# Performance work log

Hardware: AMD Instinct MI355X
Metric: run time of the kernel (lower is better)

Reference implementation:

```python
import jax, jax.numpy as jnp
import numpy as np

B, T, C = 2, 2048, 1024
H = 16
D = C // H  # head_dim = 64
SCALE = D ** -0.5


def setup_inputs() -> dict:
    key = jax.random.key(0)
    ks = jax.random.split(key, 5)
    s = 0.02
    return {
        "x": jax.random.normal(ks[0], (B, T, C), dtype=jnp.float32),
        "w_qkv": jax.random.normal(ks[1], (C, 3 * C), dtype=jnp.float32) * s,
        "b_qkv": jnp.zeros((3 * C,), dtype=jnp.float32),
        "w_proj": jax.random.normal(ks[2], (C, C), dtype=jnp.float32) * s,
        "b_proj": jnp.zeros((C,), dtype=jnp.float32),
    }


def reference(x, w_qkv, b_qkv, w_proj, b_proj):
    Bx, Tx, Cx = x.shape
    qkv = x @ w_qkv + b_qkv                      # [B,T,3C]
    q, k, v = jnp.split(qkv, 3, axis=-1)
    # [B,T,C] -> [B,H,T,D]
    q = q.reshape(Bx, Tx, H, D).transpose(0, 2, 1, 3)
    k = k.reshape(Bx, Tx, H, D).transpose(0, 2, 1, 3)
    v = v.reshape(Bx, Tx, H, D).transpose(0, 2, 1, 3)
    attn = jnp.einsum('bhqd,bhkd->bhqk', q, k) * SCALE
    causal = jnp.tril(jnp.ones((Tx, Tx), dtype=bool))
    attn = jnp.where(causal[None, None], attn, -jnp.inf)
    attn = jax.nn.softmax(attn, axis=-1)
    out = jnp.einsum('bhqk,bhkd->bhqd', attn, v)  # [B,H,T,D]
    out = out.transpose(0, 2, 1, 3).reshape(Bx, Tx, Cx)
    return out @ w_proj + b_proj
```

## Files before the change

### kernel.cpp

```cpp
#include <hip/hip_runtime.h>
#include <hip/hip_bf16.h>
#include <math.h>

#define T_SEQ 2048
#define NHEAD 16
#define HDIM  64
#define CDIM  1024
#define KDIM  1024
#define SCALE_L2E 0.1803368801111204f

typedef __attribute__((ext_vector_type(8))) short bf16x8;
typedef __attribute__((ext_vector_type(4))) float f32x4;
typedef __attribute__((ext_vector_type(16))) float f32x16;
typedef __attribute__((ext_vector_type(8))) unsigned short u16x8;
typedef __attribute__((ext_vector_type(4))) unsigned int u32x4;

__device__ __forceinline__ unsigned short f2bf(float f) {
    unsigned int u = __builtin_bit_cast(unsigned int, f);
    u += 0x7fffu + ((u >> 16) & 1u);
    return (unsigned short)(u >> 16);
}
__device__ __forceinline__ unsigned int cvt_pk_bf16(float lo, float hi_) {
    unsigned int r;
    asm("v_cvt_pk_bf16_f32 %0, %1, %2" : "=v"(r) : "v"(lo), "v"(hi_));
    return r;
}
__device__ __forceinline__ void pl32swap(unsigned int &a, unsigned int &b) {
    asm("v_permlane32_swap_b32 %0, %1" : "+v"(a), "+v"(b));
}
__device__ __forceinline__ void gld16(const unsigned short* g, unsigned short* l) {
    __builtin_amdgcn_global_load_lds(
        (const __attribute__((address_space(1))) unsigned int*)g,
        (__attribute__((address_space(3))) unsigned int*)l,
        16, 0, 0);
}

__global__ __launch_bounds__(256) void prep_all(
    const float* __restrict__ x,  unsigned short* __restrict__ Xb,
    const float* __restrict__ wq, unsigned short* __restrict__ Wqt,
    const float* __restrict__ wp, unsigned short* __restrict__ Wpt)
{
    __shared__ unsigned short Ls[64][72];
    const int bid = blockIdx.x;
    if (bid < 2048) {
        size_t i = ((size_t)bid * 256 + threadIdx.x) * 8;
        float4 a = *(const float4*)(x + i);
        float4 b = *(const float4*)(x + i + 4);
        u32x4 o;
        o[0] = cvt_pk_bf16(a.x, a.y);
        o[1] = cvt_pk_bf16(a.z, a.w);
        o[2] = cvt_pk_bf16(b.x, b.y);
        o[3] = cvt_pk_bf16(b.z, b.w);
        *(u32x4*)(Xb + i) = o;
        return;
    }
    const float* W; unsigned short* Wt; int NC, n0, k0;
    if (bid < 2048 + 768) {
        int b = bid - 2048;
        W = wq; Wt = Wqt; NC = 3072; n0 = (b % 48) * 64; k0 = (b / 48) * 64;
    } else {
        int b = bid - 2816;
        W = wp; Wt = Wpt; NC = 1024; n0 = (b % 16) * 64; k0 = (b / 16) * 64;
    }
    const int t = threadIdx.x;
    {
        int kr = t >> 2, nc = (t & 3) * 16;
        #pragma unroll
        for (int j = 0; j < 4; j++) {
            float4 v = *(const float4*)(W + (size_t)(k0 + kr) * NC + n0 + nc + j * 4);
            Ls[nc + j*4 + 0][kr] = f2bf(v.x);
            Ls[nc + j*4 + 1][kr] = f2bf(v.y);
            Ls[nc + j*4 + 2][kr] = f2bf(v.z);
            Ls[nc + j*4 + 3][kr] = f2bf(v.w);
        }
    }
    __syncthreads();
    {
        int nr = t >> 2, kc = (t & 3) * 16;
        u16x8 o0 = *(const u16x8*)&Ls[nr][kc];
        u16x8 o1 = *(const u16x8*)&Ls[nr][kc + 8];
        *(u16x8*)(Wt + (size_t)(n0 + nr) * KDIM + k0 + kc)     = o0;
        *(u16x8*)(Wt + (size_t)(n0 + nr) * KDIM + k0 + kc + 8) = o1;
    }
}

template<int NC, int EPI>
__global__ __launch_bounds__(256) void gemm_k(
    const unsigned short* __restrict__ A, const unsigned short* __restrict__ Wt,
    const float* __restrict__ bias, float* __restrict__ Of,
    unsigned short* __restrict__ Qb, unsigned short* __restrict__ Kb,
    unsigned short* __restrict__ Vt)
{
    __shared__ unsigned short As[128 * 64];
    __shared__ unsigned short Bs[128 * 64];

    const int tid  = threadIdx.x;
    const int lane = tid & 63;
    const int wid  = tid >> 6;
    const int m0 = blockIdx.x * 128;
    const int n0 = blockIdx.y * 128;
    const int wm = (wid >> 1) * 64;
    const int wn = (wid & 1) * 64;
    const int rl = lane & 15;

    const int r8 = lane >> 3, s8 = lane & 7;
    const int swzs = (s8 ^ r8) * 8;

    f32x4 acc[4][4] = {};

    for (int k0 = 0; k0 < KDIM; k0 += 64) {
        #pragma unroll
        for (int c = 0; c < 4; c++) {
            int row = (wid << 5) + (c << 3) + r8;
            gld16(A  + (size_t)(m0 + row) * KDIM + k0 + swzs, &As[(size_t)((wid<<5)+(c<<3)) * 64]);
            gld16(Wt + (size_t)(n0 + row) * KDIM + k0 + swzs, &Bs[(size_t)((wid<<5)+(c<<3)) * 64]);
        }
        __syncthreads();
        #pragma unroll
        for (int kc = 0; kc < 2; kc++) {
            const int sb = kc * 4 + (lane >> 4);
            bf16x8 af[4], bfr[4];
            #pragma unroll
            for (int f = 0; f < 4; f++) {
                int sw = (sb ^ (rl & 7)) * 8;
                af[f]  = *(const bf16x8*)&As[(wm + f*16 + rl) * 64 + sw];
                bfr[f] = *(const bf16x8*)&Bs[(wn + f*16 + rl) * 64 + sw];
            }
            __builtin_amdgcn_s_setprio(1);
            #pragma unroll
            for (int i = 0; i < 4; i++)
                #pragma unroll
                for (int j = 0; j < 4; j++)
                    acc[i][j] = __builtin_amdgcn_mfma_f32_16x16x32_bf16(af[i], bfr[j], acc[i][j], 0, 0, 0);
            __builtin_amdgcn_s_setprio(0);
        }
        __syncthreads();
    }

    #pragma unroll
    for (int j = 0; j < 4; j++) {
        int gn = n0 + wn + j*16 + rl;
        float bv = bias[gn];
        #pragma unroll
        for (int i = 0; i < 4; i++) {
            int gm0 = m0 + wm + i*16 + (lane >> 4) * 4;
            #pragma unroll
            for (int r = 0; r < 4; r++) {
                float v = acc[i][j][r] + bv;
                int gm = gm0 + r;
                if (EPI == 0) {
                    int which = gn >> 10;
                    int cw = gn & 1023;
                    int h = cw >> 6, d = cw & 63;
                    int b = gm >> 11, t = gm & 2047;
                    size_t bh = (size_t)(b * NHEAD + h);
                    if (which == 0)      Qb[(bh * T_SEQ + t) * HDIM + d] = f2bf(v * SCALE_L2E);
                    else if (which == 1) Kb[(bh * T_SEQ + t) * HDIM + d] = f2bf(v);
                    else                 Vt[(bh * HDIM + d) * T_SEQ + t] = f2bf(v);
                } else {
                    Of[(size_t)gm * NC + gn] = v;
                }
            }
        }
    }
}

__global__ __launch_bounds__(256, 4) void attn_k(
    const unsigned short* __restrict__ Qb, const unsigned short* __restrict__ Kb,
    const unsigned short* __restrict__ Vt, unsigned short* __restrict__ AO)
{
    __shared__ unsigned short sbuf[4 * 4096];
    __shared__ float mlbuf[2 * 64];

    const int tid  = threadIdx.x;
    const int lane = tid & 63;
    const int w    = tid >> 6;
    const int pair = w >> 1;
    const int par  = w & 1;
    const int bh   = blockIdx.x;
    const int by   = blockIdx.y;
    const int qt   = pair ? (63 - by) : by;
    const int ql   = lane & 31;
    const int hi   = lane >> 5;
    const int qg   = (qt << 5) + ql;

    const unsigned short* Qp = Qb + (size_t)bh * T_SEQ * HDIM;
    const unsigned short* Kp = Kb + (size_t)bh * T_SEQ * HDIM;
    const unsigned short* Vp = Vt + (size_t)bh * HDIM * T_SEQ;

    unsigned short* kbuf = sbuf + w * 4096;
    const char* kbB = (const char*)kbuf;
    const char* vbB = (const char*)(kbuf + 2048);

    const int r8 = lane >> 3, s8 = lane & 7;
    const int key = s8 ^ r8;
    const unsigned short* kSrc = Kp + (size_t)r8 * HDIM + (key << 3);
    const unsigned short* vSrc = Vp + (size_t)((key >> 2) * 32 + r8) * T_SEQ + (key & 3) * 8;

    auto issue_tile = [&](int t) {
        #pragma unroll
        for (int c = 0; c < 4; c++)
            gld16(kSrc + ((size_t)t << 11) + (c << 9), kbuf + (c << 9));
        #pragma unroll
        for (int c = 0; c < 4; c++)
            gld16(vSrc + ((size_t)c << 14) + (t << 5), kbuf + 2048 + (c << 9));
    };

    bf16x8 qf[4];
    #pragma unroll
    for (int dc = 0; dc < 4; dc++)
        qf[dc] = *(const bf16x8*)(Qp + (size_t)qg * HDIM + dc*16 + hi*8);

    float l_run = 0.f;
    f32x16 o0 = {}, o1 = {};

    if (par <= qt) {
        issue_tile(par);
        for (int t = par; t <= qt; t += 2) {
            asm volatile("s_waitcnt vmcnt(0)" ::: "memory");
            __builtin_amdgcn_sched_barrier(0);

            bf16x8 kf[4];
            #pragma unroll
            for (int dc = 0; dc < 4; dc++)
                kf[dc] = *(const bf16x8*)(kbB + ql*128 + (((dc << 1 | hi) ^ (ql & 7)) << 4));
            bf16x8 v00 = *(const bf16x8*)(vbB + ql*128 + (((0 + hi) ^ (ql & 7)) << 4));
            bf16x8 v01 = *(const bf16x8*)(vbB + ql*128 + (((2 + hi) ^ (ql & 7)) << 4));
            bf16x8 v10 = *(const bf16x8*)(vbB + ql*128 + (((4 + hi) ^ (ql & 7)) << 4));
            bf16x8 v11 = *(const bf16x8*)(vbB + ql*128 + (((6 + hi) ^ (ql & 7)) << 4));
            asm volatile("s_waitcnt lgkmcnt(0)" ::: "memory");
            __builtin_amdgcn_sched_barrier(0);

            if (t + 2 <= qt) issue_tile(t + 2);

            f32x16 s = {};
            __builtin_amdgcn_s_setprio(1);
            #pragma unroll
            for (int dc = 0; dc < 4; dc++)
                s = __builtin_amdgcn_mfma_f32_32x32x16_bf16(kf[dc], qf[dc], s, 0, 0, 0);
            __builtin_amdgcn_s_setprio(0);

            float p[16];
            if (t == qt) {
                #pragma unroll
                for (int r = 0; r < 16; r++) {
                    int kv = (t << 5) + (r & 3) + 8 * (r >> 2) + 4 * hi;
                    p[r] = (kv > qg) ? 0.f : exp2f(s[r]);
                }
            } else {
                #pragma unroll
                for (int r = 0; r < 16; r++) p[r] = exp2f(s[r]);
            }
            float r0 = (p[0]  + p[1])  + (p[2]  + p[3]);
            float r1 = (p[4]  + p[5])  + (p[6]  + p[7]);
            float r2 = (p[8]  + p[9])  + (p[10] + p[11]);
            float r3 = (p[12] + p[13]) + (p[14] + p[15]);
            l_run += (r0 + r1) + (r2 + r3);

            unsigned int c[8];
            #pragma unroll
            for (int i = 0; i < 8; i++) c[i] = cvt_pk_bf16(p[2*i], p[2*i+1]);
            pl32swap(c[0], c[2]);  pl32swap(c[1], c[3]);
            pl32swap(c[4], c[6]);  pl32swap(c[5], c[7]);
            u32x4 b0 = {c[0], c[1], c[2], c[3]};
            u32x4 b1 = {c[4], c[5], c[6], c[7]};
            bf16x8 pf0 = __builtin_bit_cast(bf16x8, b0);
            bf16x8 pf1 = __builtin_bit_cast(bf16x8, b1);

            __builtin_amdgcn_s_setprio(1);
            o0 = __builtin_amdgcn_mfma_f32_32x32x16_bf16(v00, pf0, o0, 0, 0, 0);
            o0 = __builtin_amdgcn_mfma_f32_32x32x16_bf16(v01, pf1, o0, 0, 0, 0);
            o1 = __builtin_amdgcn_mfma_f32_32x32x16_bf16(v10, pf0, o1, 0, 0, 0);
            o1 = __builtin_amdgcn_mfma_f32_32x32x16_bf16(v11, pf1, o1, 0, 0, 0);
            __builtin_amdgcn_s_setprio(0);
        }
    }

    __syncthreads();
    float* plf = (float*)(sbuf + pair * 8192);
    if (par == 1) {
        #pragma unroll
        for (int j = 0; j < 4; j++) {
            f32x4 a = { o0[4*j], o0[4*j+1], o0[4*j+2], o0[4*j+3] };
            *(f32x4*)(plf + (size_t)(j*64 + lane) * 4) = a;
        }
        #pragma unroll
        for (int j = 0; j < 4; j++) {
            f32x4 a = { o1[4*j], o1[4*j+1], o1[4*j+2], o1[4*j+3] };
            *(f32x4*)(plf + (size_t)((4+j)*64 + lane) * 4) = a;
        }
        mlbuf[pair * 64 + lane] = l_run;
    }
    __syncthreads();
    if (par == 0) {
        float l_all = l_run + mlbuf[pair * 64 + lane];
        l_all += __shfl_xor(l_all, 32);
        float linv = 1.f / l_all;
        const int b = bh >> 4, h = bh & 15;
        unsigned short* aop = AO + ((size_t)(b * T_SEQ + qg)) * CDIM + h * HDIM;
        #pragma unroll
        for (int qd = 0; qd < 4; qd++) {
            f32x4 x0 = *(const f32x4*)(plf + (size_t)(qd*64 + lane) * 4);
            f32x4 x1 = *(const f32x4*)(plf + (size_t)((4+qd)*64 + lane) * 4);
            uint2 w0, w1;
            w0.x = cvt_pk_bf16((o0[4*qd+0] + x0[0]) * linv, (o0[4*qd+1] + x0[1]) * linv);
            w0.y = cvt_pk_bf16((o0[4*qd+2] + x0[2]) * linv, (o0[4*qd+3] + x0[3]) * linv);
            w1.x = cvt_pk_bf16((o1[4*qd+0] + x1[0]) * linv, (o1[4*qd+1] + x1[1]) * linv);
            w1.y = cvt_pk_bf16((o1[4*qd+2] + x1[2]) * linv, (o1[4*qd+3] + x1[3]) * linv);
            *(uint2*)(aop + qd*8 + hi*4)      = w0;
            *(uint2*)(aop + 32 + qd*8 + hi*4) = w1;
        }
    }
}

extern "C" void kernel_launch(void* const* d_in, const int* in_sizes, int n_in,
                              void* d_out, int out_size, void* d_ws, size_t ws_size,
                              hipStream_t stream) {
    const float* x      = (const float*)d_in[0];
    const float* w_qkv  = (const float*)d_in[1];
    const float* b_qkv  = (const float*)d_in[2];
    const float* w_proj = (const float*)d_in[3];
    const float* b_proj = (const float*)d_in[4];
    float* out = (float*)d_out;

    const size_t MI = (size_t)1 << 20;
    unsigned short* base = (unsigned short*)d_ws;
    unsigned short* Qb  = base;
    unsigned short* Kb  = base + 4*MI;
    unsigned short* Vt  = base + 8*MI;
    unsigned short* Wqt = base + 12*MI;
    unsigned short* Wpt = base + 15*MI;
    unsigned short* Xb  = base + 16*MI;
    unsigned short* AO  = Xb;

    prep_all<<<dim3(3072), 256, 0, stream>>>(x, Xb, w_qkv, Wqt, w_proj, Wpt);
    gemm_k<3072, 0><<<dim3(32, 24), 256, 0, stream>>>(
        Xb, Wqt, b_qkv, nullptr, Qb, Kb, Vt);
    attn_k<<<dim3(32, 32), 256, 0, stream>>>(Qb, Kb, Vt, AO);
    gemm_k<1024, 1><<<dim3(32, 8), 256, 0, stream>>>(
        AO, Wpt, b_proj, out, nullptr, nullptr, nullptr);
}
```

Baseline: 110.0 us.

## Triple-buffer GEMM shared-memory tiles with async prefetch two stages ahead

Replaces the single-buffered K=64 GEMM main loop with a three-slot ring of K=32 shared-memory tiles. Global-to-LDS loads are issued two stages ahead and gated by explicit vmcnt waits and barriers, so memory latency overlaps with MFMA work and one barrier per iteration is removed. The swizzle is re-derived for the 32-wide rows. Each barrier now covers half as much compute, and the hand-written vmcnt accounting has to match the number of loads in flight exactly.

```diff
diff --git a/kernel.cpp b/kernel.cpp
--- a/kernel.cpp
+++ b/kernel.cpp
@@ -91,8 +91,8 @@
     unsigned short* __restrict__ Qb, unsigned short* __restrict__ Kb,
     unsigned short* __restrict__ Vt)
 {
-    __shared__ unsigned short As[128 * 64];
-    __shared__ unsigned short Bs[128 * 64];
+    __shared__ unsigned short As3[3 * 128 * 32];
+    __shared__ unsigned short Bs3[3 * 128 * 32];
 
     const int tid  = threadIdx.x;
     const int lane = tid & 63;
@@ -103,39 +103,56 @@
     const int wn = (wid & 1) * 64;
     const int rl = lane & 15;
 
-    const int r8 = lane >> 3, s8 = lane & 7;
-    const int swzs = (s8 ^ r8) * 8;
+    const int rOff   = lane >> 2;
+    const int srcOff = ((lane & 3) ^ ((lane >> 3) & 3)) * 8;
+
+    auto stage = [&](int t) {
+        const int k0 = t << 5;
+        #pragma unroll
+        for (int i = 0; i < 2; i++) {
+            int rb = (wid << 5) + (i << 4);
+            gld16(A  + (size_t)(m0 + rb + rOff) * KDIM + k0 + srcOff, &As3[(t % 3) * 4096 + rb * 32]);
+            gld16(Wt + (size_t)(n0 + rb + rOff) * KDIM + k0 + srcOff, &Bs3[(t % 3) * 4096 + rb * 32]);
+        }
+    };
 
     f32x4 acc[4][4] = {};
-
-    for (int k0 = 0; k0 < KDIM; k0 += 64) {
-        #pragma unroll
-        for (int c = 0; c < 4; c++) {
-            int row = (wid << 5) + (c << 3) + r8;
-            gld16(A  + (size_t)(m0 + row) * KDIM + k0 + swzs, &As[(size_t)((wid<<5)+(c<<3)) * 64]);
-            gld16(Wt + (size_t)(n0 + row) * KDIM + k0 + swzs, &Bs[(size_t)((wid<<5)+(c<<3)) * 64]);
-        }
-        __syncthreads();
-        #pragma unroll
-        for (int kc = 0; kc < 2; kc++) {
-            const int sb = kc * 4 + (lane >> 4);
-            bf16x8 af[4], bfr[4];
-            #pragma unroll
-            for (int f = 0; f < 4; f++) {
-                int sw = (sb ^ (rl & 7)) * 8;
-                af[f]  = *(const bf16x8*)&As[(wm + f*16 + rl) * 64 + sw];
-                bfr[f] = *(const bf16x8*)&Bs[(wn + f*16 + rl) * 64 + sw];
-            }
-            __builtin_amdgcn_s_setprio(1);
-            #pragma unroll
-            for (int i = 0; i < 4; i++)
-                #pragma unroll
-                for (int j = 0; j < 4; j++)
-                    acc[i][j] = __builtin_amdgcn_mfma_f32_16x16x32_bf16(af[i], bfr[j], acc[i][j], 0, 0, 0);
-            __builtin_amdgcn_s_setprio(0);
-        }
-        __syncthreads();
-    }
+    const int sw = ((lane >> 4) ^ ((rl >> 1) & 3)) * 8;
+
+    auto compute = [&](int t) {
+        const unsigned short* ab = &As3[(t % 3) * 4096];
+        const unsigned short* bb = &Bs3[(t % 3) * 4096];
+        bf16x8 af[4], bfr[4];
+        #pragma unroll
+        for (int f = 0; f < 4; f++) {
+            af[f]  = *(const bf16x8*)(ab + (wm + f*16 + rl) * 32 + sw);
+            bfr[f] = *(const bf16x8*)(bb + (wn + f*16 + rl) * 32 + sw);
+        }
+        __builtin_amdgcn_s_setprio(1);
+        #pragma unroll
+        for (int i = 0; i < 4; i++)
+            #pragma unroll
+            for (int j = 0; j < 4; j++)
+                acc[i][j] = __builtin_amdgcn_mfma_f32_16x16x32_bf16(af[i], bfr[j], acc[i][j], 0, 0, 0);
+        __builtin_amdgcn_s_setprio(0);
+    };
+
+    stage(0);
+    stage(1);
+    for (int ks = 0; ks < 30; ks++) {
+        asm volatile("s_waitcnt vmcnt(4)" ::: "memory");
+        __builtin_amdgcn_s_barrier();
+        __builtin_amdgcn_sched_barrier(0);
+        stage(ks + 2);
+        compute(ks);
+        __builtin_amdgcn_sched_barrier(0);
+    }
+    asm volatile("s_waitcnt vmcnt(4)" ::: "memory");
+    __builtin_amdgcn_s_barrier();
+    compute(30);
+    asm volatile("s_waitcnt vmcnt(0)" ::: "memory");
+    __builtin_amdgcn_s_barrier();
+    compute(31);
 
     #pragma unroll
     for (int j = 0; j < 4; j++) {
```

Measured after the change: 113.6 us. 3.3% more time.
